# Kernel tuning notes

Measured on AMD Instinct MI355X. Metric: run time of the kernel, lower is better.

Reference implementation:

```python
import jax, jax.numpy as jnp
import numpy as np

C = 128          # feature channels
N = 1_048_576    # octree nodes at depth 6 (divisible by 8)
M = 262_144      # full parent node count at depth 5 (incl. empty nodes)


def setup_inputs() -> dict:
    key = jax.random.key(0)
    k1, k2, k3 = jax.random.split(key, 3)
    data = jax.random.normal(k1, (C, N), dtype=jnp.float32)
    idx = jax.random.randint(k2, (M,), 0, N // 8, dtype=jnp.int32)
    empty = jax.random.uniform(k3, (M,)) < 0.5
    child_idx = jnp.where(empty, jnp.int32(-1), idx)  # -1 => empty (zero pad)
    return {"data": data, "child_idx": child_idx}


def reference(data, child_idx):
    # octree_max_pool: every 8 consecutive sibling nodes -> 1 parent value
    c, n = data.shape
    grouped = data.reshape(c, n // 8, 8)          # [C, N/8, 8]
    pooled = grouped.max(axis=-1)                  # [C, N/8]
    # octree_pad: scatter pooled non-empty parents into full parent node list,
    # zero-filling empty nodes (child_idx == -1).
    safe = jnp.clip(child_idx, 0, None)            # safe gather index
    out = jnp.where(child_idx[None, :] >= 0, pooled[:, safe], jnp.float32(0))
    return out                                     # [C, M]
```

## Files before the change

### kernel.cpp

```cpp
#include <hip/hip_runtime.h>


#define CH 128
#define CH_PER_BLOCK 8

__global__ __launch_bounds__(256) void pool_kernel(
    const float* __restrict__ data,
    float* __restrict__ pooled,
    int total_groups)
{
    int g = blockIdx.x * 256 + threadIdx.x;
    if (g >= total_groups) return;
    const float4* p = (const float4*)(data + (size_t)g * 8);
    float4 a = p[0];
    float4 b = p[1];
    pooled[g] = fmaxf(fmaxf(fmaxf(a.x, a.y), fmaxf(a.z, a.w)),
                      fmaxf(fmaxf(b.x, b.y), fmaxf(b.z, b.w)));
}

__global__ __launch_bounds__(256) void pad_kernel(
    const float* __restrict__ pooled,
    const int* __restrict__ child_idx,
    float* __restrict__ out,
    int groups_per_ch,
    int m_total)
{
    int m = blockIdx.x * 256 + threadIdx.x;
    if (m >= m_total) return;
    int idx = child_idx[m];
    int c0 = blockIdx.y * CH_PER_BLOCK;

    if (idx < 0) {
        #pragma unroll
        for (int cc = 0; cc < CH_PER_BLOCK; ++cc)
            out[(size_t)(c0 + cc) * m_total + m] = 0.0f;
    } else {
        #pragma unroll
        for (int cc = 0; cc < CH_PER_BLOCK; ++cc)
            out[(size_t)(c0 + cc) * m_total + m] =
                pooled[(size_t)(c0 + cc) * groups_per_ch + idx];
    }
}

__global__ __launch_bounds__(256) void fused_kernel(
    const float* __restrict__ data,
    const int* __restrict__ child_idx,
    float* __restrict__ out,
    int n, int m_total)
{
    int m = blockIdx.x * 256 + threadIdx.x;
    if (m >= m_total) return;
    int idx = child_idx[m];
    int c0 = blockIdx.y * CH_PER_BLOCK;
    if (idx < 0) {
        #pragma unroll
        for (int cc = 0; cc < CH_PER_BLOCK; ++cc)
            out[(size_t)(c0 + cc) * m_total + m] = 0.0f;
        return;
    }
    size_t base = (size_t)idx * 8;
    #pragma unroll
    for (int cc = 0; cc < CH_PER_BLOCK; ++cc) {
        const float4* p = (const float4*)(data + (size_t)(c0 + cc) * n + base);
        float4 a = p[0];
        float4 b = p[1];
        out[(size_t)(c0 + cc) * m_total + m] =
            fmaxf(fmaxf(fmaxf(a.x, a.y), fmaxf(a.z, a.w)),
                  fmaxf(fmaxf(b.x, b.y), fmaxf(b.z, b.w)));
    }
}

extern "C" void kernel_launch(void* const* d_in, const int* in_sizes, int n_in,
                              void* d_out, int out_size, void* d_ws, size_t ws_size,
                              hipStream_t stream) {
    const float* data      = (const float*)d_in[0];
    const int*   child_idx = (const int*)d_in[1];
    float*       out       = (float*)d_out;

    int n = in_sizes[0] / CH;
    int m = in_sizes[1];
    int gpc = n / 8;
    int total_groups = CH * gpc;
    size_t pooled_bytes = (size_t)total_groups * sizeof(float);

    if (ws_size >= pooled_bytes) {
        float* pooled = (float*)d_ws;
        dim3 b1(256), g1((total_groups + 255) / 256);
        hipLaunchKernelGGL(pool_kernel, g1, b1, 0, stream, data, pooled, total_groups);
        dim3 b2(256), g2((m + 255) / 256, CH / CH_PER_BLOCK);
        hipLaunchKernelGGL(pad_kernel, g2, b2, 0, stream, pooled, child_idx, out, gpc, m);
    } else {
        dim3 b(256), g((m + 255) / 256, CH / CH_PER_BLOCK);
        hipLaunchKernelGGL(fused_kernel, g, b, 0, stream, data, child_idx, out, n, m);
    }
}
```

Before: 833.6 us.

## Store pooled intermediate channel-innermost so pad gathers contiguous records

The pool kernel now writes pooled values in a transposed [group][channel] layout. Each thread reduces four channels for one group and writes them as a float4. The pad kernel then reads a contiguous 128-byte slice of the record per gathered index and handles 32 channels per thread, instead of doing one 4-byte random gather per channel. This removes the scattered per-channel reads from the pooled buffer. The cost is strided channel-row reads in the pool kernel and higher register use per thread in the pad kernel.

```diff
diff --git a/kernel.cpp b/kernel.cpp
--- a/kernel.cpp
+++ b/kernel.cpp
@@ -2,43 +2,61 @@
 
 
 #define CH 128
-#define CH_PER_BLOCK 8
 
-__global__ __launch_bounds__(256) void pool_kernel(
+__global__ __launch_bounds__(256) void pool_t_kernel(
     const float* __restrict__ data,
-    float* __restrict__ pooled,
-    int total_groups)
+    float* __restrict__ pooled_t,
+    int n,
+    int gpc)
 {
-    int g = blockIdx.x * 256 + threadIdx.x;
-    if (g >= total_groups) return;
-    const float4* p = (const float4*)(data + (size_t)g * 8);
-    float4 a = p[0];
-    float4 b = p[1];
-    pooled[g] = fmaxf(fmaxf(fmaxf(a.x, a.y), fmaxf(a.z, a.w)),
-                      fmaxf(fmaxf(b.x, b.y), fmaxf(b.z, b.w)));
+    int t  = threadIdx.x;
+    int gl = t >> 5;
+    int cq = t & 31;
+    int g  = blockIdx.x * 8 + gl;
+    if (g >= gpc) return;
+    int c0 = cq * 4;
+
+    const float* base = data + (size_t)g * 8;
+    float v[4];
+    #pragma unroll
+    for (int k = 0; k < 4; ++k) {
+        const float4* p = (const float4*)(base + (size_t)(c0 + k) * n);
+        float4 a = p[0];
+        float4 b = p[1];
+        v[k] = fmaxf(fmaxf(fmaxf(a.x, a.y), fmaxf(a.z, a.w)),
+                     fmaxf(fmaxf(b.x, b.y), fmaxf(b.z, b.w)));
+    }
+    *(float4*)(pooled_t + (size_t)g * CH + c0) = make_float4(v[0], v[1], v[2], v[3]);
 }
 
-__global__ __launch_bounds__(256) void pad_kernel(
-    const float* __restrict__ pooled,
+__global__ __launch_bounds__(256) void pad_t_kernel(
+    const float* __restrict__ pooled_t,
     const int* __restrict__ child_idx,
     float* __restrict__ out,
-    int groups_per_ch,
     int m_total)
 {
     int m = blockIdx.x * 256 + threadIdx.x;
     if (m >= m_total) return;
     int idx = child_idx[m];
-    int c0 = blockIdx.y * CH_PER_BLOCK;
+    int c0 = blockIdx.y * 32;
 
     if (idx < 0) {
         #pragma unroll
-        for (int cc = 0; cc < CH_PER_BLOCK; ++cc)
-            out[(size_t)(c0 + cc) * m_total + m] = 0.0f;
-    } else {
-        #pragma unroll
-        for (int cc = 0; cc < CH_PER_BLOCK; ++cc)
-            out[(size_t)(c0 + cc) * m_total + m] =
-                pooled[(size_t)(c0 + cc) * groups_per_ch + idx];
+        for (int k = 0; k < 32; ++k)
+            out[(size_t)(c0 + k) * m_total + m] = 0.0f;
+        return;
+    }
+
+    const float4* rec = (const float4*)(pooled_t + (size_t)idx * CH + c0);
+    float4 v[8];
+    #pragma unroll
+    for (int k = 0; k < 8; ++k) v[k] = rec[k];
+    #pragma unroll
+    for (int k = 0; k < 8; ++k) {
+        out[(size_t)(c0 + 4 * k + 0) * m_total + m] = v[k].x;
+        out[(size_t)(c0 + 4 * k + 1) * m_total + m] = v[k].y;
+        out[(size_t)(c0 + 4 * k + 2) * m_total + m] = v[k].z;
+        out[(size_t)(c0 + 4 * k + 3) * m_total + m] = v[k].w;
     }
 }
 
@@ -51,16 +69,16 @@
     int m = blockIdx.x * 256 + threadIdx.x;
     if (m >= m_total) return;
     int idx = child_idx[m];
-    int c0 = blockIdx.y * CH_PER_BLOCK;
+    int c0 = blockIdx.y * 8;
     if (idx < 0) {
         #pragma unroll
-        for (int cc = 0; cc < CH_PER_BLOCK; ++cc)
+        for (int cc = 0; cc < 8; ++cc)
             out[(size_t)(c0 + cc) * m_total + m] = 0.0f;
         return;
     }
     size_t base = (size_t)idx * 8;
     #pragma unroll
-    for (int cc = 0; cc < CH_PER_BLOCK; ++cc) {
+    for (int cc = 0; cc < 8; ++cc) {
         const float4* p = (const float4*)(data + (size_t)(c0 + cc) * n + base);
         float4 a = p[0];
         float4 b = p[1];
@@ -77,20 +95,19 @@
     const int*   child_idx = (const int*)d_in[1];
     float*       out       = (float*)d_out;
 
-    int n = in_sizes[0] / CH;
-    int m = in_sizes[1];
+    int n   = in_sizes[0] / CH;
+    int m   = in_sizes[1];
     int gpc = n / 8;
-    int total_groups = CH * gpc;
-    size_t pooled_bytes = (size_t)total_groups * sizeof(float);
+    size_t pooled_bytes = (size_t)gpc * CH * sizeof(float);
 
     if (ws_size >= pooled_bytes) {
-        float* pooled = (float*)d_ws;
-        dim3 b1(256), g1((total_groups + 255) / 256);
-        hipLaunchKernelGGL(pool_kernel, g1, b1, 0, stream, data, pooled, total_groups);
-        dim3 b2(256), g2((m + 255) / 256, CH / CH_PER_BLOCK);
-        hipLaunchKernelGGL(pad_kernel, g2, b2, 0, stream, pooled, child_idx, out, gpc, m);
+        float* pooled_t = (float*)d_ws;
+        dim3 b1(256), g1((gpc + 7) / 8);
+        hipLaunchKernelGGL(pool_t_kernel, g1, b1, 0, stream, data, pooled_t, n, gpc);
+        dim3 b2(256), g2((m + 255) / 256, 4);
+        hipLaunchKernelGGL(pad_t_kernel, g2, b2, 0, stream, pooled_t, child_idx, out, m);
     } else {
-        dim3 b(256), g((m + 255) / 256, CH / CH_PER_BLOCK);
+        dim3 b(256), g((m + 255) / 256, CH / 8);
         hipLaunchKernelGGL(fused_kernel, g, b, 0, stream, data, child_idx, out, n, m);
     }
 }
```

New measurement: 805.2 us. 3.4% less time.
